# Performance work log

Hardware: AMD Instinct MI355X
Metric: run time of the kernel (lower is better)

## Reference

```python
import jax, jax.numpy as jnp
import numpy as np

N_CAM = 6
N_HEADS = 8
N_POINTS = 4
D = 256  # internal d_model of the deformable attention


def _sine_pos(h, w, d=D):
    # DETR PositionEmbeddingSine, normalize=True, channels-last (h, w, d)
    npf = d // 2
    two_pi = 2.0 * np.pi
    y = jnp.arange(1, h + 1, dtype=jnp.float32) / (h + 1e-6) * two_pi
    x = jnp.arange(1, w + 1, dtype=jnp.float32) / (w + 1e-6) * two_pi
    dim_t = (10000.0 ** (2.0 * (jnp.arange(npf) // 2) / npf)).astype(jnp.float32)
    def enc(v):
        p = v[:, None] / dim_t
        return jnp.stack([jnp.sin(p[:, 0::2]), jnp.cos(p[:, 1::2])], axis=-1).reshape(v.shape[0], -1)
    py, px = enc(y), enc(x)
    return jnp.concatenate([
        jnp.broadcast_to(py[:, None, :], (h, w, npf)),
        jnp.broadcast_to(px[None, :, :], (h, w, npf))], axis=-1)


def _layernorm(x, g, b, eps=1e-5):
    mu = jnp.mean(x, -1, keepdims=True)
    var = jnp.mean((x - mu) ** 2, -1, keepdims=True)
    return (x - mu) * jax.lax.rsqrt(var + eps) * g + b


def _bilinear_gather(kv, loc_x, loc_y, H, W):
    # kv: (b, L, heads, H*W, c); loc_*: (b, Lq, heads, L, P) normalized to [0,1]
    # emulates F.grid_sample(mode='bilinear', padding_mode='zeros', align_corners=False)
    b, L, heads, HW, c = kv.shape
    _, Lq, _, _, P = loc_x.shape
    x = loc_x * W - 0.5
    y = loc_y * H - 0.5
    x0 = jnp.floor(x)
    y0 = jnp.floor(y)
    fx = x - x0
    fy = y - y0
    out = jnp.zeros((b, Lq, heads, L, P, c), kv.dtype)
    for dx in (0, 1):
        for dy in (0, 1):
            xi = x0 + dx
            yi = y0 + dy
            valid = (xi >= 0) & (xi < W) & (yi >= 0) & (yi < H)
            wgt = (fx if dx else 1.0 - fx) * (fy if dy else 1.0 - fy) * valid
            idx = (jnp.clip(yi, 0, H - 1) * W + jnp.clip(xi, 0, W - 1)).astype(jnp.int32)
            idx_t = idx.transpose(0, 3, 2, 1, 4).reshape(b, L, heads, Lq * P, 1)
            g = jnp.take_along_axis(kv, idx_t, axis=3)
            g = g.reshape(b, L, heads, Lq, P, c).transpose(0, 3, 2, 1, 4, 5)
            out = out + wgt[..., None] * g
    return out  # (b, Lq, heads, L, P, c)


def reference(x, conv0_w, conv0_b, conv2_w, conv2_b, cam_emb,
              off_w, off_b, val_w, val_b, key_w, key_b, out_w, out_b,
              conv1_w, conv1_b, norm0_g, norm0_b,
              lin1_w, lin1_b, lin2_w, lin2_b, norm2_g, norm2_b):
    bn, dim, H, W = x.shape
    b = bn // N_CAM
    hd = D // N_HEADS
    HW = H * W
    Lq = N_CAM * HW

    x_nhwc = x.transpose(0, 2, 3, 1)                  # (bn, H, W, dim)
    residual = x_nhwc.reshape(b, Lq, dim)             # b (n h w) d

    src = (x_nhwc @ conv0_w.T + conv0_b).reshape(b, N_CAM, H, W, D)  # conv0 1x1

    pos = _sine_pos(H, W)                              # (H, W, 256)
    spc = src + pos[None, None] + cam_emb[None, :, None, None, :]
    # per-level global descriptor: mean over pixels of conv2(src+pos+cam)
    g = jnp.mean((spc @ conv2_w.T + conv2_b).reshape(b, N_CAM, HW, D), axis=2)  # (b, n, 256)

    src_flat = src.reshape(b, Lq, D)
    query = spc.reshape(b, Lq, D)                      # src + cam + pos (flattened)

    value = src_flat @ val_w.T + val_b
    keys = src_flat @ key_w.T + key_b

    # sampling locations: per-query reference point + learned offsets (normalized)
    offsets = (query @ off_w.T + off_b).reshape(b, Lq, N_HEADS, N_CAM, N_POINTS, 2)
    ry, rx = jnp.meshgrid(
        (jnp.arange(H, dtype=jnp.float32) + 0.5) / H,
        (jnp.arange(W, dtype=jnp.float32) + 0.5) / W, indexing='ij')
    ref = jnp.tile(jnp.stack([rx.ravel(), ry.ravel()], -1), (N_CAM, 1))  # (Lq, 2) as (x, y)
    loc = ref[None, :, None, None, None, :] + offsets / jnp.array([W, H], jnp.float32)

    # gather keys and values in a single bilinear pass (concat on channel)
    kv = jnp.concatenate([
        keys.reshape(b, N_CAM, HW, N_HEADS, hd),
        value.reshape(b, N_CAM, HW, N_HEADS, hd)], axis=-1).transpose(0, 1, 3, 2, 4)
    sampled = _bilinear_gather(kv, loc[..., 0], loc[..., 1], H, W)  # (b,Lq,heads,L,P,2hd)
    k_s, v_s = sampled[..., :hd], sampled[..., hd:]

    # append per-level global token as an extra key/value point per level
    g_h = g.reshape(b, 1, N_CAM, N_HEADS, hd).transpose(0, 1, 3, 2, 4)[:, :, :, :, None, :]
    g_h = jnp.broadcast_to(g_h, (b, Lq, N_HEADS, N_CAM, 1, hd))
    k_all = jnp.concatenate([k_s, g_h], axis=4)        # (b,Lq,heads,L,P+1,hd)
    v_all = jnp.concatenate([v_s, g_h], axis=4)

    # key-aware attention: softmax over all (level, point) sampled keys
    q_h = query.reshape(b, Lq, N_HEADS, hd)
    logits = jnp.einsum('bqhd,bqhlpd->bqhlp', q_h, k_all) / jnp.sqrt(jnp.float32(hd))
    attn = jax.nn.softmax(logits.reshape(b, Lq, N_HEADS, -1), axis=-1).reshape(logits.shape)
    attn_out = jnp.einsum('bqhlp,bqhlpd->bqhd', attn, v_all).reshape(b, Lq, D)
    attn_out = attn_out @ out_w.T + out_b

    out = attn_out @ conv1_w.T + conv1_b               # conv1 1x1 back to dim
    out = _layernorm(residual + out, norm0_g, norm0_b)
    ffn = jax.nn.relu(out @ lin1_w.T + lin1_b) @ lin2_w.T + lin2_b
    out = _layernorm(out + ffn, norm2_g, norm2_b)

    return out.reshape(b, N_CAM, H, W, dim).transpose(0, 1, 4, 2, 3).reshape(bn, dim, H, W)


def setup_inputs() -> dict:
    key = jax.random.key(0)
    ks = jax.random.split(key, 16)
    B, DIM, H, W = 1, 256, 20, 40

    def w(k, shape, s=0.02):
        return jax.random.normal(k, shape, jnp.float32) * s

    n_off = N_HEADS * N_CAM * N_POINTS * 2
    return {
        "x": jax.random.normal(ks[0], (B * N_CAM, DIM, H, W), jnp.float32),
        "conv0_w": w(ks[1], (D, DIM)), "conv0_b": jnp.zeros((D,), jnp.float32),
        "conv2_w": w(ks[2], (D, D)), "conv2_b": jnp.zeros((D,), jnp.float32),
        "cam_emb": jax.random.uniform(ks[3], (N_CAM, D), jnp.float32),
        "off_w": w(ks[4], (n_off, D)),
        "off_b": jax.random.normal(ks[5], (n_off,), jnp.float32) * 0.5,
        "val_w": w(ks[6], (D, D)), "val_b": jnp.zeros((D,), jnp.float32),
        "key_w": w(ks[7], (D, D)), "key_b": jnp.zeros((D,), jnp.float32),
        "out_w": w(ks[8], (D, D)), "out_b": jnp.zeros((D,), jnp.float32),
        "conv1_w": w(ks[9], (DIM, D)), "conv1_b": jnp.zeros((DIM,), jnp.float32),
        "norm0_g": jnp.ones((DIM,), jnp.float32), "norm0_b": jnp.zeros((DIM,), jnp.float32),
        "lin1_w": w(ks[10], (DIM, DIM)), "lin1_b": jnp.zeros((DIM,), jnp.float32),
        "lin2_w": w(ks[11], (DIM, DIM)), "lin2_b": jnp.zeros((DIM,), jnp.float32),
        "norm2_g": jnp.ones((DIM,), jnp.float32), "norm2_b": jnp.zeros((DIM,), jnp.float32),
    }
```

## Files before the change

### kernel.cpp

```cpp
#include <hip/hip_runtime.h>
#include <math.h>

typedef unsigned short u16;
typedef unsigned int u32;

#define NCAM 6
#define NHEADS 8
#define NPOINTS 4
#define DD 256
#define HH 20
#define WW 40
#define HWSZ 800
#define LQ 4800
#define HDIM 32

typedef __attribute__((ext_vector_type(8))) short bf16x8;
typedef __attribute__((ext_vector_type(4))) float f32x4;

__device__ __forceinline__ u16 f2b(float x) {
    union { float f; u32 u; } v;
    v.f = x;
    u32 r = (v.u + 0x7FFFu + ((v.u >> 16) & 1u)) >> 16;
    return (u16)r;
}
__device__ __forceinline__ float lo2f(u32 u) {
    union { u32 u; float f; } v; v.u = u << 16; return v.f;
}
__device__ __forceinline__ float hi2f(u32 u) {
    union { u32 u; float f; } v; v.u = u & 0xFFFF0000u; return v.f;
}

#define P1_BLOCKS 3698
__global__ __launch_bounds__(256) void prep1(
    const float* __restrict__ x, const float* __restrict__ conv0_w,
    const float* __restrict__ conv0_b, const float* __restrict__ key_w,
    const float* __restrict__ key_b, const float* __restrict__ val_w,
    const float* __restrict__ val_b, const float* __restrict__ off_w,
    const float* __restrict__ off_b, const float* __restrict__ lin1_w,
    const float* __restrict__ lin2_w, const float* __restrict__ conv1_w,
    const float* __restrict__ conv1_b, const float* __restrict__ out_w,
    const float* __restrict__ out_b, const float* __restrict__ cam_emb,
    float* __restrict__ pos, u16* __restrict__ xtb, float* __restrict__ mu_x,
    u16* __restrict__ Wcat, float* __restrict__ bias_cat,
    u16* __restrict__ lin1b, u16* __restrict__ lin2b,
    u16* __restrict__ wcombb, float* __restrict__ bcomb,
    float* __restrict__ camoff, float* __restrict__ posy,
    float* __restrict__ posx) {
    int b = blockIdx.x, t = threadIdx.x;
    if (b < 800) {
        int hw = b, d = t;
        int h = hw / WW, w = hw % WW;
        int j = (d & 127) >> 1;
        float dim = powf(10000.0f, (float)j * (1.0f / 64.0f));
        float v;
        if (d < 128) v = (float)(h + 1) / (20.0f + 1e-6f) * (2.0f * (float)M_PI);
        else         v = (float)(w + 1) / (40.0f + 1e-6f) * (2.0f * (float)M_PI);
        float p = v / dim;
        pos[hw * DD + d] = (d & 1) ? cosf(p) : sinf(p);
    } else if (b < 1184) {
        int row = (b - 800) * 4 + (t >> 6);
        int lane = t & 63;
        const float* base = x + (size_t)row * HWSZ;
        float s = 0.f;
        for (int i = lane; i < HWSZ; i += 64) s += base[i];
#pragma unroll
        for (int m = 1; m <= 32; m <<= 1) s += __shfl_xor(s, m);
        if (lane == 0) mu_x[row] = s * (1.0f / (float)HWSZ);
    } else if (b < 1952) {
        int i = (b - 1184) * 256 + t;
        if (i < 65536) {
            Wcat[i] = f2b(conv0_w[i]);
            if (i < 256) bias_cat[i] = conv0_b[i];
        } else if (i < 131072) {
            lin1b[i - 65536] = f2b(lin1_w[i - 65536]);
        } else {
            lin2b[i - 131072] = f2b(lin2_w[i - 131072]);
        }
    } else if (b < 2176) {
        int rbase = 256 + (b - 1952) * 4;
        __shared__ float rowv[4][DD];
        __shared__ float cb[DD];
        cb[t] = conv0_b[t];
#pragma unroll
        for (int j = 0; j < 4; ++j) {
            int row = rbase + j;
            const float* srcp;
            if (row < 768) {
                int rj = row - 256;
                int head = rj >> 6, cpair = (rj >> 1) & 31, kv = rj & 1;
                srcp = (kv ? val_w : key_w) + (size_t)(head * 32 + cpair) * DD;
            } else {
                srcp = off_w + (size_t)(row - 768) * DD;
            }
            rowv[j][t] = srcp[t];
        }
        __syncthreads();
        float acc[4] = {0.f, 0.f, 0.f, 0.f};
        for (int c = 0; c < DD; ++c) {
            float w0 = conv0_w[(size_t)c * DD + t];
#pragma unroll
            for (int j = 0; j < 4; ++j) acc[j] += rowv[j][c] * w0;
        }
#pragma unroll
        for (int j = 0; j < 4; ++j) Wcat[(size_t)(rbase + j) * DD + t] = f2b(acc[j]);
        if (t < 4) {
            int row = rbase + t;
            float bb;
            if (row < 768) {
                int rj = row - 256;
                int head = rj >> 6, cpair = (rj >> 1) & 31, kv = rj & 1;
                bb = (kv ? val_b : key_b)[head * 32 + cpair];
            } else {
                bb = off_b[row - 768];
            }
            for (int c = 0; c < DD; ++c) bb += rowv[t][c] * cb[c];
            bias_cat[row] = bb;
        }
    } else if (b < 2432) {
        int n = b - 2176;
        __shared__ float rowv[DD];
        rowv[t] = conv1_w[(size_t)n * DD + t];
        __syncthreads();
        float acc = 0.f;
        for (int m = 0; m < DD; ++m) acc += rowv[m] * out_w[(size_t)m * DD + t];
        wcombb[(size_t)n * DD + t] = f2b(acc);
        if (t == 0) {
            float bb = conv1_b[n];
            for (int m = 0; m < DD; ++m) bb += rowv[m] * out_b[m];
            bcomb[n] = bb;
        }
    } else if (b < 2438) {
        int cam = b - 2432;
        __shared__ float ce[DD];
        ce[t] = cam_emb[cam * DD + t];
        __syncthreads();
        for (int i = t; i < 384; i += 256) {
            float a = 0.f;
            const float* wr = off_w + (size_t)i * DD;
            for (int c = 0; c < DD; ++c) a += ce[c] * wr[c];
            camoff[cam * 384 + i] = a;
        }
    } else if (b < 2498) {
        int idx = b - 2438;
        __shared__ float pv[128];
        int yside = (idx < 20);
        int coord = yside ? idx : idx - 20;
        if (t < 128) {
            int d = t, j = d >> 1;
            float dim = powf(10000.0f, (float)j * (1.0f / 64.0f));
            float v = yside
                ? (float)(coord + 1) / (20.0f + 1e-6f) * (2.0f * (float)M_PI)
                : (float)(coord + 1) / (40.0f + 1e-6f) * (2.0f * (float)M_PI);
            float p = v / dim;
            pv[d] = (d & 1) ? cosf(p) : sinf(p);
        }
        __syncthreads();
        int koff = yside ? 0 : 128;
        float* outp = yside ? (posy + coord * 384) : (posx + coord * 384);
        for (int n = t; n < 384; n += 256) {
            const float* wr = off_w + (size_t)n * DD + koff;
            float a = 0.f;
            for (int d = 0; d < 128; ++d) a += pv[d] * wr[d];
            outp[n] = a;
        }
    } else {
        int idx = b - 2498;
        int cam = idx / 200, rem = idx % 200;
        int hw0 = (rem % 25) * 32, c0 = (rem / 25) * 32;
        __shared__ float tile[32][33];
        int lhw = t & 31, lc4 = t >> 5;
#pragma unroll
        for (int i = 0; i < 4; ++i) {
            int lc = lc4 * 4 + i;
            tile[lc][lhw] = x[((size_t)(cam * DD + c0 + lc)) * HWSZ + hw0 + lhw];
        }
        __syncthreads();
        int lc2 = t & 31, lhw4 = t >> 5;
#pragma unroll
        for (int i = 0; i < 4; ++i) {
            int lhw2 = lhw4 * 4 + i;
            xtb[((size_t)(cam * HWSZ + hw0 + lhw2)) * DD + c0 + lc2] =
                f2b(tile[lc2][lhw2]);
        }
    }
}

__global__ __launch_bounds__(256) void gemm_fused(
    const u16* __restrict__ Ab, const u16* __restrict__ Wcat,
    const float* __restrict__ bias_cat, const float* __restrict__ pos,
    const float* __restrict__ cam_emb, u16* __restrict__ spcb,
    u16* __restrict__ kvcat16, float* __restrict__ offs,
    const float* __restrict__ mu_x, const float* __restrict__ conv0_w,
    const float* __restrict__ conv0_b, const float* __restrict__ conv2_w,
    const float* __restrict__ conv2_b, float* __restrict__ g) {
    int b = blockIdx.x, t = threadIdx.x;
    if (b < 1350) {
        __shared__ __align__(16) u16 As[1056];
        __shared__ __align__(16) u16 Bs[4120];
        int col0 = (b % 9) * 128, row0 = (b / 9) * 32;
        int wv = t >> 6, lane = t & 63;
        int quad = lane >> 4, l = lane & 15;
        f32x4 acc[2][2] = {};
        for (int k0 = 0; k0 < 256; k0 += 32) {
            __syncthreads();
            if (t < 128) {
                int m = t >> 2, j = t & 3;
                *(uint4*)&As[(j * 33 + m) * 8] =
                    *(const uint4*)&Ab[(size_t)(row0 + m) * 256 + k0 + j * 8];
            }
            {
                int n = t >> 1, jp = (t & 1) * 2;
                const u16* gsrc = &Wcat[(size_t)(col0 + n) * 256 + k0 + jp * 8];
                *(uint4*)&Bs[(jp * 129 + n) * 8]       = *(const uint4*)gsrc;
                *(uint4*)&Bs[((jp + 1) * 129 + n) * 8] = *(const uint4*)(gsrc + 8);
            }
            __syncthreads();
            bf16x8 a0 = *(const bf16x8*)&As[(quad * 33 + l) * 8];
            bf16x8 a1 = *(const bf16x8*)&As[(quad * 33 + 16 + l) * 8];
            bf16x8 b0 = *(const bf16x8*)&Bs[(quad * 129 + wv * 32 + l) * 8];
            bf16x8 b1 = *(const bf16x8*)&Bs[(quad * 129 + wv * 32 + 16 + l) * 8];
            acc[0][0] = __builtin_amdgcn_mfma_f32_16x16x32_bf16(a0, b0, acc[0][0], 0, 0, 0);
            acc[0][1] = __builtin_amdgcn_mfma_f32_16x16x32_bf16(a0, b1, acc[0][1], 0, 0, 0);
            acc[1][0] = __builtin_amdgcn_mfma_f32_16x16x32_bf16(a1, b0, acc[1][0], 0, 0, 0);
            acc[1][1] = __builtin_amdgcn_mfma_f32_16x16x32_bf16(a1, b1, acc[1][1], 0, 0, 0);
        }
#pragma unroll
        for (int mt = 0; mt < 2; ++mt) {
#pragma unroll
            for (int nt = 0; nt < 2; ++nt) {
                int col = col0 + wv * 32 + nt * 16 + l;
                float bb = bias_cat[col];
#pragma unroll
                for (int r = 0; r < 4; ++r) {
                    int row = row0 + mt * 16 + quad * 4 + r;
                    float v = acc[mt][nt][r] + bb;
                    if (col0 < 256) {
                        int cam = row / HWSZ, hw = row % HWSZ;
                        spcb[(size_t)row * 256 + col] =
                            f2b(v + pos[(size_t)hw * 256 + col] + cam_emb[cam * 256 + col]);
                    } else if (col0 < 768) {
                        kvcat16[(size_t)row * 512 + (col - 256)] = f2b(v);
                    } else {
                        offs[(size_t)row * 384 + (col - 768)] = v;
                    }
                }
            }
        }
    } else {
        int cam = b - 1350;
        __shared__ float mu[DD];
        __shared__ float smu[DD];
        float pm;
        {
            int d = t;
            int j = (d & 127) >> 1;
            float inv = 1.0f / powf(10000.0f, (float)j * (1.0f / 64.0f));
            float s = 0.f;
            if (d < 128) {
                for (int h = 0; h < HH; ++h) {
                    float p = (float)(h + 1) / (20.0f + 1e-6f) * (2.0f * (float)M_PI) * inv;
                    s += (d & 1) ? cosf(p) : sinf(p);
                }
                pm = s * (1.0f / (float)HH);
            } else {
                for (int w = 0; w < WW; ++w) {
                    float p = (float)(w + 1) / (40.0f + 1e-6f) * (2.0f * (float)M_PI) * inv;
                    s += (d & 1) ? cosf(p) : sinf(p);
                }
                pm = s * (1.0f / (float)WW);
            }
        }
        mu[t] = mu_x[cam * DD + t];
        __syncthreads();
        float a = conv0_b[t] + pm + cam_emb[cam * DD + t];
        const float* wr = conv0_w + (size_t)t * DD;
        for (int k = 0; k < DD; ++k) a += mu[k] * wr[k];
        smu[t] = a;
        __syncthreads();
        float ga = conv2_b[t];
        const float* w2r = conv2_w + (size_t)t * DD;
        for (int d = 0; d < DD; ++d) ga += smu[d] * w2r[d];
        g[cam * DD + t] = ga;
    }
}

__global__ __launch_bounds__(256, 6) void attn_kernel(
    const u16* __restrict__ spcb, const u16* __restrict__ kvcat16,
    const float* __restrict__ offs, const float* __restrict__ posy,
    const float* __restrict__ posx, const float* __restrict__ camoff,
    const float* __restrict__ g, u16* __restrict__ attn_out) {
    int qq = blockIdx.x;
    int q0 = qq * 2;
    int tid = threadIdx.x;
    int cam = q0 / HWSZ;
    int hw0 = q0 % HWSZ;
    __shared__ float soff[2][384];
    __shared__ float wgt[2][192][4];
    __shared__ int   idxp[2][192][4];
    for (int i = tid; i < 768; i += 256) {
        int qi = i / 384, n = i - qi * 384;
        int hw = hw0 + qi;
        int h = hw / WW, w = hw - h * WW;
        soff[qi][n] = offs[(size_t)(q0 + qi) * 384 + n] + posy[h * 384 + n] +
                      posx[w * 384 + n] + camoff[cam * 384 + n];
    }
    __syncthreads();
    for (int e2 = tid; e2 < 384; e2 += 256) {
        int qi = e2 / 192, e = e2 - qi * 192;
        int head = e / 24, r = e - head * 24;
        int scam = r >> 2;
        int hw = hw0 + qi;
        int h = hw / WW, w = hw - h * WW;
        float X = (float)w + soff[qi][e * 2];
        float Y = (float)h + soff[qi][e * 2 + 1];
        float x0f = floorf(X), y0f = floorf(Y);
        float fx = X - x0f, fy = Y - y0f;
        int x0 = (int)x0f, y0 = (int)y0f, x1 = x0 + 1, y1 = y0 + 1;
        float vx0 = (x0 >= 0 && x0 < WW) ? 1.f : 0.f;
        float vx1 = (x1 >= 0 && x1 < WW) ? 1.f : 0.f;
        float vy0 = (y0 >= 0 && y0 < HH) ? 1.f : 0.f;
        float vy1 = (y1 >= 0 && y1 < HH) ? 1.f : 0.f;
        int cx0 = min(max(x0, 0), WW - 1), cx1 = min(max(x1, 0), WW - 1);
        int cy0 = min(max(y0, 0), HH - 1), cy1 = min(max(y1, 0), HH - 1);
        wgt[qi][e][0] = (1.f - fx) * (1.f - fy) * vx0 * vy0;
        wgt[qi][e][1] = fx * (1.f - fy) * vx1 * vy0;
        wgt[qi][e][2] = (1.f - fx) * fy * vx0 * vy1;
        wgt[qi][e][3] = fx * fy * vx1 * vy1;
        int pb = scam * HWSZ, hb = head * 64;
        idxp[qi][e][0] = ((pb + cy0 * WW + cx0) << 9) + hb;
        idxp[qi][e][1] = ((pb + cy0 * WW + cx1) << 9) + hb;
        idxp[qi][e][2] = ((pb + cy1 * WW + cx0) << 9) + hb;
        idxp[qi][e][3] = ((pb + cy1 * WW + cx1) << 9) + hb;
    }
    __syncthreads();
    int qi = tid >> 7, head = (tid >> 4) & 7, l = tid & 15;
    int q = q0 + qi;
    int c0 = l * 2;
    u32 qu = *(const u32*)&spcb[(size_t)q * 256 + head * 32 + c0];
    const float scale = 0.17677669529663687f;
    float q0s = lo2f(qu) * scale, q1s = hi2f(qu) * scale;
    float m = -1e30f, den = 0.f, o0 = 0.f, o1 = 0.f;
    for (int sc = 0; sc < NCAM; ++sc) {
        float av0[4], av1[4], lg[4];
#pragma unroll
        for (int p = 0; p < 4; ++p) {
            int e = head * 24 + sc * 4 + p;
            float ak0 = 0.f, ak1 = 0.f, a0 = 0.f, a1 = 0.f;
#pragma unroll
            for (int j = 0; j < 4; ++j) {
                float wj = wgt[qi][e][j];
                int idx = idxp[qi][e][j] + 4 * l;
                uint2 d = *(const uint2*)&kvcat16[idx];
                ak0 += wj * lo2f(d.x);
                a0  += wj * hi2f(d.x);
                ak1 += wj * lo2f(d.y);
                a1  += wj * hi2f(d.y);
            }
            av0[p] = a0; av1[p] = a1;
            float pl = q0s * ak0 + q1s * ak1;
            pl += __shfl_xor(pl, 1);
            pl += __shfl_xor(pl, 2);
            pl += __shfl_xor(pl, 4);
            pl += __shfl_xor(pl, 8);
            lg[p] = pl;
        }
        float2 gv = *(const float2*)&g[sc * 256 + head * 32 + c0];
        float pg = q0s * gv.x + q1s * gv.y;
        pg += __shfl_xor(pg, 1);
        pg += __shfl_xor(pg, 2);
        pg += __shfl_xor(pg, 4);
        pg += __shfl_xor(pg, 8);
        float mc = fmaxf(fmaxf(fmaxf(lg[0], lg[1]), fmaxf(lg[2], lg[3])), pg);
        float mn = fmaxf(m, mc);
        float aa = __expf(m - mn);
        float e0p = __expf(lg[0] - mn), e1p = __expf(lg[1] - mn);
        float e2p = __expf(lg[2] - mn), e3p = __expf(lg[3] - mn);
        float e4p = __expf(pg - mn);
        den = den * aa + (e0p + e1p + e2p + e3p + e4p);
        o0 = o0 * aa + e0p * av0[0] + e1p * av0[1] + e2p * av0[2] + e3p * av0[3] + e4p * gv.x;
        o1 = o1 * aa + e0p * av1[0] + e1p * av1[1] + e2p * av1[2] + e3p * av1[3] + e4p * gv.y;
        m = mn;
    }
    float inv = 1.f / den;
    u32 pack = (u32)f2b(o0 * inv) | ((u32)f2b(o1 * inv) << 16);
    *(u32*)&attn_out[(size_t)q * 256 + head * 32 + c0] = pack;
}

__global__ __launch_bounds__(256) void epilogue(
    const u16* __restrict__ Ab, const u16* __restrict__ Wc,
    const float* __restrict__ bcomb, const float* __restrict__ x_nchw,
    const float* __restrict__ n0g, const float* __restrict__ n0b,
    const u16* __restrict__ W1, const float* __restrict__ b1v,
    const u16* __restrict__ W2, const float* __restrict__ b2v,
    const float* __restrict__ n2g, const float* __restrict__ n2b,
    float* __restrict__ out_nchw) {
    __shared__ __align__(16) u16 As[552];
    __shared__ __align__(16) u16 Bs[8232];
    __shared__ __align__(16) u16 A2[4360];
    __shared__ float red[4][4][4][2];
    int t = threadIdx.x;
    int row0 = blockIdx.x * 16;
    int wv = t >> 6, lane = t & 63, quad = lane >> 4, l = lane & 15;
    int cam = row0 / HWSZ;
    int hw0q = row0 % HWSZ + quad * 4;

    f32x4 acc[4] = {};
    for (int k0 = 0; k0 < 256; k0 += 32) {
        __syncthreads();
        if (t < 64) {
            int mm = t >> 2, j = t & 3;
            *(uint4*)&As[(j * 17 + mm) * 8] =
                *(const uint4*)&Ab[(size_t)(row0 + mm) * 256 + k0 + j * 8];
        }
#pragma unroll
        for (int j = 0; j < 4; ++j)
            *(uint4*)&Bs[(j * 257 + t) * 8] =
                *(const uint4*)&Wc[(size_t)t * 256 + k0 + j * 8];
        __syncthreads();
        bf16x8 a = *(const bf16x8*)&As[(quad * 17 + l) * 8];
#pragma unroll
        for (int nt = 0; nt < 4; ++nt) {
            bf16x8 b = *(const bf16x8*)&Bs[(quad * 257 + wv * 64 + nt * 16 + l) * 8];
            acc[nt] = __builtin_amdgcn_mfma_f32_16x16x32_bf16(a, b, acc[nt], 0, 0, 0);
        }
    }
    float v[4][4];
    int cols[4];
#pragma unroll
    for (int nt = 0; nt < 4; ++nt) {
        int col = wv * 64 + nt * 16 + l;
        cols[nt] = col;
        float bb = bcomb[col];
        float4 rx = *(const float4*)&x_nchw[((size_t)(cam * 256 + col)) * HWSZ + hw0q];
        v[nt][0] = acc[nt][0] + bb + rx.x;
        v[nt][1] = acc[nt][1] + bb + rx.y;
        v[nt][2] = acc[nt][2] + bb + rx.z;
        v[nt][3] = acc[nt][3] + bb + rx.w;
    }
#pragma unroll
    for (int r = 0; r < 4; ++r) {
        float s = v[0][r] + v[1][r] + v[2][r] + v[3][r];
        float sq = v[0][r] * v[0][r] + v[1][r] * v[1][r] +
                   v[2][r] * v[2][r] + v[3][r] * v[3][r];
#pragma unroll
        for (int msk = 1; msk <= 8; msk <<= 1) {
            s += __shfl_xor(s, msk);
            sq += __shfl_xor(sq, msk);
        }
        if (l == 0) { red[wv][quad][r][0] = s; red[wv][quad][r][1] = sq; }
    }
    __syncthreads();
    float o0[4][4];
#pragma unroll
    for (int r = 0; r < 4; ++r) {
        float S = red[0][quad][r][0] + red[1][quad][r][0] +
                  red[2][quad][r][0] + red[3][quad][r][0];
        float Q = red[0][quad][r][1] + red[1][quad][r][1] +
                  red[2][quad][r][1] + red[3][quad][r][1];
        float mean = S * (1.0f / 256.0f);
        float var = Q * (1.0f / 256.0f) - mean * mean;
        float rstd = rsqrtf(var + 1e-5f);
        int row = quad * 4 + r;
#pragma unroll
        for (int nt = 0; nt < 4; ++nt) {
            int col = cols[nt];
            float ov = (v[nt][r] - mean) * rstd * n0g[col] + n0b[col];
            o0[nt][r] = ov;
            A2[((col >> 3) * 17 + row) * 8 + (col & 7)] = f2b(ov);
        }
    }
    f32x4 acc2[4] = {};
    for (int k0 = 0; k0 < 256; k0 += 32) {
        __syncthreads();
#pragma unroll
        for (int j = 0; j < 4; ++j)
            *(uint4*)&Bs[(j * 257 + t) * 8] =
                *(const uint4*)&W1[(size_t)t * 256 + k0 + j * 8];
        __syncthreads();
        bf16x8 a = *(const bf16x8*)&A2[(((k0 >> 3) + quad) * 17 + l) * 8];
#pragma unroll
        for (int nt = 0; nt < 4; ++nt) {
            bf16x8 b = *(const bf16x8*)&Bs[(quad * 257 + wv * 64 + nt * 16 + l) * 8];
            acc2[nt] = __builtin_amdgcn_mfma_f32_16x16x32_bf16(a, b, acc2[nt], 0, 0, 0);
        }
    }
    __syncthreads();
#pragma unroll
    for (int nt = 0; nt < 4; ++nt) {
        int col = cols[nt];
        float bb = b1v[col];
#pragma unroll
        for (int r = 0; r < 4; ++r) {
            int row = quad * 4 + r;
            A2[((col >> 3) * 17 + row) * 8 + (col & 7)] = f2b(fmaxf(acc2[nt][r] + bb, 0.f));
        }
    }
    f32x4 acc3[4] = {};
    for (int k0 = 0; k0 < 256; k0 += 32) {
        __syncthreads();
#pragma unroll
        for (int j = 0; j < 4; ++j)
            *(uint4*)&Bs[(j * 257 + t) * 8] =
                *(const uint4*)&W2[(size_t)t * 256 + k0 + j * 8];
        __syncthreads();
        bf16x8 a = *(const bf16x8*)&A2[(((k0 >> 3) + quad) * 17 + l) * 8];
#pragma unroll
        for (int nt = 0; nt < 4; ++nt) {
            bf16x8 b = *(const bf16x8*)&Bs[(quad * 257 + wv * 64 + nt * 16 + l) * 8];
            acc3[nt] = __builtin_amdgcn_mfma_f32_16x16x32_bf16(a, b, acc3[nt], 0, 0, 0);
        }
    }
    float v2[4][4];
#pragma unroll
    for (int nt = 0; nt < 4; ++nt) {
        float bb = b2v[cols[nt]];
#pragma unroll
        for (int r = 0; r < 4; ++r) v2[nt][r] = acc3[nt][r] + bb + o0[nt][r];
    }
    __syncthreads();
#pragma unroll
    for (int r = 0; r < 4; ++r) {
        float s = v2[0][r] + v2[1][r] + v2[2][r] + v2[3][r];
        float sq = v2[0][r] * v2[0][r] + v2[1][r] * v2[1][r] +
                   v2[2][r] * v2[2][r] + v2[3][r] * v2[3][r];
#pragma unroll
        for (int msk = 1; msk <= 8; msk <<= 1) {
            s += __shfl_xor(s, msk);
            sq += __shfl_xor(sq, msk);
        }
        if (l == 0) { red[wv][quad][r][0] = s; red[wv][quad][r][1] = sq; }
    }
    __syncthreads();
    float mean2[4], rstd2[4];
#pragma unroll
    for (int r = 0; r < 4; ++r) {
        float S = red[0][quad][r][0] + red[1][quad][r][0] +
                  red[2][quad][r][0] + red[3][quad][r][0];
        float Q = red[0][quad][r][1] + red[1][quad][r][1] +
                  red[2][quad][r][1] + red[3][quad][r][1];
        mean2[r] = S * (1.0f / 256.0f);
        float var = Q * (1.0f / 256.0f) - mean2[r] * mean2[r];
        rstd2[r] = rsqrtf(var + 1e-5f);
    }
#pragma unroll
    for (int nt = 0; nt < 4; ++nt) {
        int col = cols[nt];
        float gg = n2g[col], bb = n2b[col];
        float4 ov4;
        ov4.x = (v2[nt][0] - mean2[0]) * rstd2[0] * gg + bb;
        ov4.y = (v2[nt][1] - mean2[1]) * rstd2[1] * gg + bb;
        ov4.z = (v2[nt][2] - mean2[2]) * rstd2[2] * gg + bb;
        ov4.w = (v2[nt][3] - mean2[3]) * rstd2[3] * gg + bb;
        *(float4*)&out_nchw[((size_t)(cam * 256 + col)) * HWSZ + hw0q] = ov4;
    }
}

extern "C" void kernel_launch(void* const* d_in, const int* in_sizes, int n_in,
                              void* d_out, int out_size, void* d_ws, size_t ws_size,
                              hipStream_t stream) {
    const float* x       = (const float*)d_in[0];
    const float* conv0_w = (const float*)d_in[1];
    const float* conv0_b = (const float*)d_in[2];
    const float* conv2_w = (const float*)d_in[3];
    const float* conv2_b = (const float*)d_in[4];
    const float* cam_emb = (const float*)d_in[5];
    const float* off_w   = (const float*)d_in[6];
    const float* off_b   = (const float*)d_in[7];
    const float* val_w   = (const float*)d_in[8];
    const float* val_b   = (const float*)d_in[9];
    const float* key_w   = (const float*)d_in[10];
    const float* key_b   = (const float*)d_in[11];
    const float* out_w   = (const float*)d_in[12];
    const float* out_b   = (const float*)d_in[13];
    const float* conv1_w = (const float*)d_in[14];
    const float* conv1_b = (const float*)d_in[15];
    const float* norm0_g = (const float*)d_in[16];
    const float* norm0_b = (const float*)d_in[17];
    const float* lin1_w  = (const float*)d_in[18];
    const float* lin1_b  = (const float*)d_in[19];
    const float* lin2_w  = (const float*)d_in[20];
    const float* lin2_b  = (const float*)d_in[21];
    const float* norm2_g = (const float*)d_in[22];
    const float* norm2_b = (const float*)d_in[23];

    float* ws = (float*)d_ws;
    float* pos      = ws;
    float* mu_x     = pos + 204800;
    float* g        = mu_x + 1536;
    float* camoff   = g + 1536;
    float* posy     = camoff + 2304;
    float* posx     = posy + 7680;
    float* bias_cat = posx + 15360;
    float* bcomb    = bias_cat + 1152;
    float* offs     = bcomb + 256;
    float* f_xtb    = offs + 1843200;
    float* f_spcb   = f_xtb + 614400;
    float* f_kvcat  = f_spcb + 614400;
    float* f_Wcat   = f_kvcat + 1228800;
    float* f_lin1b  = f_Wcat + 147456;
    float* f_lin2b  = f_lin1b + 32768;
    float* f_wcombb = f_lin2b + 32768;

    u16* xtb     = (u16*)f_xtb;
    u16* spcb    = (u16*)f_spcb;
    u16* kvcat16 = (u16*)f_kvcat;
    u16* Wcat    = (u16*)f_Wcat;
    u16* lin1b   = (u16*)f_lin1b;
    u16* lin2b   = (u16*)f_lin2b;
    u16* wcombb  = (u16*)f_wcombb;
    u16* attn_ob = xtb;

    prep1<<<P1_BLOCKS, 256, 0, stream>>>(
        x, conv0_w, conv0_b, key_w, key_b, val_w, val_b, off_w, off_b,
        lin1_w, lin2_w, conv1_w, conv1_b, out_w, out_b, cam_emb,
        pos, xtb, mu_x, Wcat, bias_cat, lin1b, lin2b, wcombb, bcomb,
        camoff, posy, posx);
    gemm_fused<<<1356, 256, 0, stream>>>(xtb, Wcat, bias_cat, pos, cam_emb,
                                         spcb, kvcat16, offs, mu_x, conv0_w,
                                         conv0_b, conv2_w, conv2_b, g);
    attn_kernel<<<LQ / 2, 256, 0, stream>>>(spcb, kvcat16, offs, posy, posx,
                                            camoff, g, attn_ob);
    epilogue<<<300, 256, 0, stream>>>(attn_ob, wcombb, bcomb, x,
                                      norm0_g, norm0_b, lin1b, lin1_b,
                                      lin2b, lin2_b, norm2_g, norm2_b,
                                      (float*)d_out);
}
```

Measured before the change: 220.3 us.

## Move weight folding to MFMA prep kernel, enlarge GEMM tiles, batch attention cameras

Weight folding (key/val/off rows times conv0, and conv1 times out_w) moves out of scalar per-thread loops in prep1 into a new prep2 kernel that uses bf16 MFMA on pre-converted and transposed weights. The small matvecs for camoff, posy/posx and biases now use float4 loads with a 16-lane shuffle reduction. gemm_fused tiles grow from 32 to 64 rows, halving the block count. The attention kernel processes two cameras per online-softmax step with launch bounds lowered to 4 waves, and the folded weights now pass through bf16 before folding, which adds rounding error.

```diff
diff --git a/kernel.cpp b/kernel.cpp
--- a/kernel.cpp
+++ b/kernel.cpp
@@ -29,8 +29,15 @@
 __device__ __forceinline__ float hi2f(u32 u) {
     union { u32 u; float f; } v; v.u = u & 0xFFFF0000u; return v.f;
 }
-
-#define P1_BLOCKS 3698
+__device__ __forceinline__ float red16(float s) {
+    s += __shfl_xor(s, 1);
+    s += __shfl_xor(s, 2);
+    s += __shfl_xor(s, 4);
+    s += __shfl_xor(s, 8);
+    return s;
+}
+
+#define P1_BLOCKS 4570
 __global__ __launch_bounds__(256) void prep1(
     const float* __restrict__ x, const float* __restrict__ conv0_w,
     const float* __restrict__ conv0_b, const float* __restrict__ key_w,
@@ -42,10 +49,12 @@
     const float* __restrict__ out_b, const float* __restrict__ cam_emb,
     float* __restrict__ pos, u16* __restrict__ xtb, float* __restrict__ mu_x,
     u16* __restrict__ Wcat, float* __restrict__ bias_cat,
-    u16* __restrict__ lin1b, u16* __restrict__ lin2b,
-    u16* __restrict__ wcombb, float* __restrict__ bcomb,
-    float* __restrict__ camoff, float* __restrict__ posy,
-    float* __restrict__ posx) {
+    u16* __restrict__ conv1b, u16* __restrict__ lin1b, u16* __restrict__ lin2b,
+    u16* __restrict__ off_wb, u16* __restrict__ kvpackb,
+    u16* __restrict__ conv0_wTb, u16* __restrict__ out_wTb,
+    float* __restrict__ bcomb, float* __restrict__ camoff,
+    float* __restrict__ posy, float* __restrict__ posx) {
+    __shared__ float sbuf[1088];
     int b = blockIdx.x, t = threadIdx.x;
     if (b < 800) {
         int hw = b, d = t;
@@ -66,83 +75,67 @@
 #pragma unroll
         for (int m = 1; m <= 32; m <<= 1) s += __shfl_xor(s, m);
         if (lane == 0) mu_x[row] = s * (1.0f / (float)HWSZ);
-    } else if (b < 1952) {
+    } else if (b < 3104) {
         int i = (b - 1184) * 256 + t;
         if (i < 65536) {
             Wcat[i] = f2b(conv0_w[i]);
             if (i < 256) bias_cat[i] = conv0_b[i];
         } else if (i < 131072) {
-            lin1b[i - 65536] = f2b(lin1_w[i - 65536]);
+            conv1b[i - 65536] = f2b(conv1_w[i - 65536]);
+        } else if (i < 196608) {
+            lin1b[i - 131072] = f2b(lin1_w[i - 131072]);
+        } else if (i < 262144) {
+            lin2b[i - 196608] = f2b(lin2_w[i - 196608]);
+        } else if (i < 360448) {
+            off_wb[i - 262144] = f2b(off_w[i - 262144]);
         } else {
-            lin2b[i - 131072] = f2b(lin2_w[i - 131072]);
-        }
-    } else if (b < 2176) {
-        int rbase = 256 + (b - 1952) * 4;
-        __shared__ float rowv[4][DD];
-        __shared__ float cb[DD];
-        cb[t] = conv0_b[t];
-#pragma unroll
-        for (int j = 0; j < 4; ++j) {
-            int row = rbase + j;
-            const float* srcp;
-            if (row < 768) {
-                int rj = row - 256;
-                int head = rj >> 6, cpair = (rj >> 1) & 31, kv = rj & 1;
-                srcp = (kv ? val_w : key_w) + (size_t)(head * 32 + cpair) * DD;
-            } else {
-                srcp = off_w + (size_t)(row - 768) * DD;
-            }
-            rowv[j][t] = srcp[t];
-        }
-        __syncthreads();
-        float acc[4] = {0.f, 0.f, 0.f, 0.f};
-        for (int c = 0; c < DD; ++c) {
-            float w0 = conv0_w[(size_t)c * DD + t];
-#pragma unroll
-            for (int j = 0; j < 4; ++j) acc[j] += rowv[j][c] * w0;
-        }
-#pragma unroll
-        for (int j = 0; j < 4; ++j) Wcat[(size_t)(rbase + j) * DD + t] = f2b(acc[j]);
-        if (t < 4) {
-            int row = rbase + t;
-            float bb;
-            if (row < 768) {
-                int rj = row - 256;
-                int head = rj >> 6, cpair = (rj >> 1) & 31, kv = rj & 1;
-                bb = (kv ? val_b : key_b)[head * 32 + cpair];
-            } else {
-                bb = off_b[row - 768];
-            }
-            for (int c = 0; c < DD; ++c) bb += rowv[t][c] * cb[c];
-            bias_cat[row] = bb;
-        }
-    } else if (b < 2432) {
-        int n = b - 2176;
-        __shared__ float rowv[DD];
-        rowv[t] = conv1_w[(size_t)n * DD + t];
-        __syncthreads();
-        float acc = 0.f;
-        for (int m = 0; m < DD; ++m) acc += rowv[m] * out_w[(size_t)m * DD + t];
-        wcombb[(size_t)n * DD + t] = f2b(acc);
-        if (t == 0) {
-            float bb = conv1_b[n];
-            for (int m = 0; m < DD; ++m) bb += rowv[m] * out_b[m];
-            bcomb[n] = bb;
-        }
-    } else if (b < 2438) {
-        int cam = b - 2432;
-        __shared__ float ce[DD];
-        ce[t] = cam_emb[cam * DD + t];
-        __syncthreads();
-        for (int i = t; i < 384; i += 256) {
-            float a = 0.f;
-            const float* wr = off_w + (size_t)i * DD;
-            for (int c = 0; c < DD; ++c) a += ce[c] * wr[c];
-            camoff[cam * 384 + i] = a;
-        }
-    } else if (b < 2498) {
-        int idx = b - 2438;
-        __shared__ float pv[128];
+            int j = i - 360448;
+            int rj = j >> 8, k = j & 255;
+            int head = rj >> 6, cpair = (rj >> 1) & 31, kv = rj & 1;
+            kvpackb[j] = f2b((kv ? val_w : key_w)[(size_t)(head * 32 + cpair) * 256 + k]);
+        }
+    } else if (b < 3232) {
+        int idx = b - 3104;
+        int which = idx >> 6;
+        int t2 = idx & 63;
+        int k0 = (t2 >> 3) * 32, c0 = (t2 & 7) * 32;
+        const float* src = which ? out_w : conv0_w;
+        u16* dst = which ? out_wTb : conv0_wTb;
+        float (*tile)[33] = (float(*)[33])sbuf;
+        int lc = t & 31, lk4 = t >> 5;
+#pragma unroll
+        for (int i = 0; i < 4; ++i) {
+            int lk = lk4 * 4 + i;
+            tile[lk][lc] = src[(size_t)(k0 + lk) * 256 + c0 + lc];
+        }
+        __syncthreads();
+        int lk2 = t & 31, lc4 = t >> 5;
+#pragma unroll
+        for (int i = 0; i < 4; ++i) {
+            int lc2 = lc4 * 4 + i;
+            dst[(size_t)(c0 + lc2) * 256 + k0 + lk2] = f2b(tile[lk2][lc2]);
+        }
+    } else if (b < 4432) {
+        int idx = b - 3232;
+        int cam = idx / 200, rem = idx % 200;
+        int hw0 = (rem % 25) * 32, c0 = (rem / 25) * 32;
+        float (*tile)[33] = (float(*)[33])sbuf;
+        int lhw = t & 31, lc4 = t >> 5;
+#pragma unroll
+        for (int i = 0; i < 4; ++i) {
+            int lc = lc4 * 4 + i;
+            tile[lc][lhw] = x[((size_t)(cam * DD + c0 + lc)) * HWSZ + hw0 + lhw];
+        }
+        __syncthreads();
+        int lc2 = t & 31, lhw4 = t >> 5;
+#pragma unroll
+        for (int i = 0; i < 4; ++i) {
+            int lhw2 = lhw4 * 4 + i;
+            xtb[((size_t)(cam * HWSZ + hw0 + lhw2)) * DD + c0 + lc2] =
+                f2b(tile[lc2][lhw2]);
+        }
+    } else if (b < 4492) {
+        int idx = b - 4432;
         int yside = (idx < 20);
         int coord = yside ? idx : idx - 20;
         if (t < 128) {
@@ -152,35 +145,138 @@
                 ? (float)(coord + 1) / (20.0f + 1e-6f) * (2.0f * (float)M_PI)
                 : (float)(coord + 1) / (40.0f + 1e-6f) * (2.0f * (float)M_PI);
             float p = v / dim;
-            pv[d] = (d & 1) ? cosf(p) : sinf(p);
+            sbuf[d] = (d & 1) ? cosf(p) : sinf(p);
         }
         __syncthreads();
         int koff = yside ? 0 : 128;
         float* outp = yside ? (posy + coord * 384) : (posx + coord * 384);
-        for (int n = t; n < 384; n += 256) {
-            const float* wr = off_w + (size_t)n * DD + koff;
-            float a = 0.f;
-            for (int d = 0; d < 128; ++d) a += pv[d] * wr[d];
-            outp[n] = a;
-        }
+        int l = t & 15, og = t >> 4;
+#pragma unroll
+        for (int chunk = 0; chunk < 24; ++chunk) {
+            int n = chunk * 16 + og;
+            const float* wr = off_w + (size_t)n * 256 + koff + l * 8;
+            float4 w0 = *(const float4*)wr;
+            float4 w1 = *(const float4*)(wr + 4);
+            const float* pv = sbuf + l * 8;
+            float s = pv[0] * w0.x + pv[1] * w0.y + pv[2] * w0.z + pv[3] * w0.w +
+                      pv[4] * w1.x + pv[5] * w1.y + pv[6] * w1.z + pv[7] * w1.w;
+            s = red16(s);
+            if (l == 0) outp[n] = s;
+        }
+    } else if (b < 4498) {
+        int cam = b - 4492;
+        sbuf[t] = cam_emb[cam * DD + t];
+        __syncthreads();
+        int l = t & 15, og = t >> 4;
+#pragma unroll
+        for (int chunk = 0; chunk < 24; ++chunk) {
+            int n = chunk * 16 + og;
+            const float* wr = off_w + (size_t)n * 256 + l * 16;
+            float s = 0.f;
+#pragma unroll
+            for (int i = 0; i < 4; ++i) {
+                float4 w4 = *(const float4*)(wr + i * 4);
+                const float* ce = sbuf + l * 16 + i * 4;
+                s += ce[0] * w4.x + ce[1] * w4.y + ce[2] * w4.z + ce[3] * w4.w;
+            }
+            s = red16(s);
+            if (l == 0) camoff[cam * 384 + n] = s;
+        }
+    } else if (b < 4554) {
+        sbuf[t] = conv0_b[t];
+        __syncthreads();
+        int l = t & 15, og = t >> 4;
+        int rr = (b - 4498) * 16 + og;
+        const float* srcp;
+        float bsrc;
+        if (rr < 512) {
+            int head = rr >> 6, cpair = (rr >> 1) & 31, kv = rr & 1;
+            srcp = (kv ? val_w : key_w) + (size_t)(head * 32 + cpair) * 256;
+            bsrc = (kv ? val_b : key_b)[head * 32 + cpair];
+        } else {
+            srcp = off_w + (size_t)(rr - 512) * 256;
+            bsrc = off_b[rr - 512];
+        }
+        float s = 0.f;
+#pragma unroll
+        for (int i = 0; i < 4; ++i) {
+            float4 w4 = *(const float4*)(srcp + l * 16 + i * 4);
+            const float* cb = sbuf + l * 16 + i * 4;
+            s += cb[0] * w4.x + cb[1] * w4.y + cb[2] * w4.z + cb[3] * w4.w;
+        }
+        s = red16(s);
+        if (l == 0) bias_cat[256 + rr] = bsrc + s;
     } else {
-        int idx = b - 2498;
-        int cam = idx / 200, rem = idx % 200;
-        int hw0 = (rem % 25) * 32, c0 = (rem / 25) * 32;
-        __shared__ float tile[32][33];
-        int lhw = t & 31, lc4 = t >> 5;
+        sbuf[t] = out_b[t];
+        __syncthreads();
+        int l = t & 15, og = t >> 4;
+        int n = (b - 4554) * 16 + og;
+        float s = 0.f;
 #pragma unroll
         for (int i = 0; i < 4; ++i) {
-            int lc = lc4 * 4 + i;
-            tile[lc][lhw] = x[((size_t)(cam * DD + c0 + lc)) * HWSZ + hw0 + lhw];
-        }
-        __syncthreads();
-        int lc2 = t & 31, lhw4 = t >> 5;
-#pragma unroll
-        for (int i = 0; i < 4; ++i) {
-            int lhw2 = lhw4 * 4 + i;
-            xtb[((size_t)(cam * HWSZ + hw0 + lhw2)) * DD + c0 + lc2] =
-                f2b(tile[lc2][lhw2]);
+            float4 w4 = *(const float4*)(conv1_w + (size_t)n * 256 + l * 16 + i * 4);
+            const float* ob = sbuf + l * 16 + i * 4;
+            s += ob[0] * w4.x + ob[1] * w4.y + ob[2] * w4.z + ob[3] * w4.w;
+        }
+        s = red16(s);
+        if (l == 0) bcomb[n] = conv1_b[n] + s;
+    }
+}
+
+__global__ __launch_bounds__(256) void prep2(
+    const u16* __restrict__ kvpackb, const u16* __restrict__ off_wb,
+    const u16* __restrict__ conv0_wTb, const u16* __restrict__ conv1b,
+    const u16* __restrict__ out_wTb, u16* __restrict__ Wcat,
+    u16* __restrict__ wcombb) {
+    __shared__ __align__(16) u16 As[1056];
+    __shared__ __align__(16) u16 Bs[4120];
+    int b = blockIdx.x, t = threadIdx.x;
+    int isfold = (b < 56);
+    int bb = isfold ? b : b - 56;
+    int row0 = (bb >> 1) * 32, col0 = (bb & 1) * 128;
+    const u16* Wb = isfold ? conv0_wTb : out_wTb;
+    int wv = t >> 6, lane = t & 63;
+    int quad = lane >> 4, l = lane & 15;
+    f32x4 acc[2][2] = {};
+    for (int k0 = 0; k0 < 256; k0 += 32) {
+        __syncthreads();
+        if (t < 128) {
+            int m = t >> 2, j = t & 3;
+            int rr = row0 + m;
+            const u16* ap;
+            if (isfold) ap = (rr < 512) ? (kvpackb + (size_t)rr * 256)
+                                        : (off_wb + (size_t)(rr - 512) * 256);
+            else        ap = conv1b + (size_t)rr * 256;
+            *(uint4*)&As[(j * 33 + m) * 8] = *(const uint4*)&ap[k0 + j * 8];
+        }
+        {
+            int n = t >> 1, jp = (t & 1) * 2;
+            const u16* gsrc = &Wb[(size_t)(col0 + n) * 256 + k0 + jp * 8];
+            *(uint4*)&Bs[(jp * 129 + n) * 8]       = *(const uint4*)gsrc;
+            *(uint4*)&Bs[((jp + 1) * 129 + n) * 8] = *(const uint4*)(gsrc + 8);
+        }
+        __syncthreads();
+        bf16x8 a0 = *(const bf16x8*)&As[(quad * 33 + l) * 8];
+        bf16x8 a1 = *(const bf16x8*)&As[(quad * 33 + 16 + l) * 8];
+        bf16x8 b0 = *(const bf16x8*)&Bs[(quad * 129 + wv * 32 + l) * 8];
+        bf16x8 b1 = *(const bf16x8*)&Bs[(quad * 129 + wv * 32 + 16 + l) * 8];
+        acc[0][0] = __builtin_amdgcn_mfma_f32_16x16x32_bf16(a0, b0, acc[0][0], 0, 0, 0);
+        acc[0][1] = __builtin_amdgcn_mfma_f32_16x16x32_bf16(a0, b1, acc[0][1], 0, 0, 0);
+        acc[1][0] = __builtin_amdgcn_mfma_f32_16x16x32_bf16(a1, b0, acc[1][0], 0, 0, 0);
+        acc[1][1] = __builtin_amdgcn_mfma_f32_16x16x32_bf16(a1, b1, acc[1][1], 0, 0, 0);
+    }
+#pragma unroll
+    for (int mt = 0; mt < 2; ++mt) {
+#pragma unroll
+        for (int nt = 0; nt < 2; ++nt) {
+            int col = col0 + wv * 32 + nt * 16 + l;
+#pragma unroll
+            for (int r = 0; r < 4; ++r) {
+                int rr = row0 + mt * 16 + quad * 4 + r;
+                u16 ov = f2b(acc[mt][nt][r]);
+                if (isfold) Wcat[(size_t)(256 + rr) * 256 + col] = ov;
+                else        wcombb[(size_t)rr * 256 + col] = ov;
+            }
         }
     }
 }
@@ -194,18 +290,18 @@
     const float* __restrict__ conv0_b, const float* __restrict__ conv2_w,
     const float* __restrict__ conv2_b, float* __restrict__ g) {
     int b = blockIdx.x, t = threadIdx.x;
-    if (b < 1350) {
-        __shared__ __align__(16) u16 As[1056];
+    if (b < 675) {
+        __shared__ __align__(16) u16 As[2080];
         __shared__ __align__(16) u16 Bs[4120];
-        int col0 = (b % 9) * 128, row0 = (b / 9) * 32;
+        int col0 = (b % 9) * 128, row0 = (b / 9) * 64;
         int wv = t >> 6, lane = t & 63;
         int quad = lane >> 4, l = lane & 15;
-        f32x4 acc[2][2] = {};
+        f32x4 acc[4][2] = {};
         for (int k0 = 0; k0 < 256; k0 += 32) {
             __syncthreads();
-            if (t < 128) {
+            {
                 int m = t >> 2, j = t & 3;
-                *(uint4*)&As[(j * 33 + m) * 8] =
+                *(uint4*)&As[(j * 65 + m) * 8] =
                     *(const uint4*)&Ab[(size_t)(row0 + m) * 256 + k0 + j * 8];
             }
             {
@@ -215,17 +311,17 @@
                 *(uint4*)&Bs[((jp + 1) * 129 + n) * 8] = *(const uint4*)(gsrc + 8);
             }
             __syncthreads();
-            bf16x8 a0 = *(const bf16x8*)&As[(quad * 33 + l) * 8];
-            bf16x8 a1 = *(const bf16x8*)&As[(quad * 33 + 16 + l) * 8];
             bf16x8 b0 = *(const bf16x8*)&Bs[(quad * 129 + wv * 32 + l) * 8];
             bf16x8 b1 = *(const bf16x8*)&Bs[(quad * 129 + wv * 32 + 16 + l) * 8];
-            acc[0][0] = __builtin_amdgcn_mfma_f32_16x16x32_bf16(a0, b0, acc[0][0], 0, 0, 0);
-            acc[0][1] = __builtin_amdgcn_mfma_f32_16x16x32_bf16(a0, b1, acc[0][1], 0, 0, 0);
-            acc[1][0] = __builtin_amdgcn_mfma_f32_16x16x32_bf16(a1, b0, acc[1][0], 0, 0, 0);
-            acc[1][1] = __builtin_amdgcn_mfma_f32_16x16x32_bf16(a1, b1, acc[1][1], 0, 0, 0);
-        }
-#pragma unroll
-        for (int mt = 0; mt < 2; ++mt) {
+#pragma unroll
+            for (int mt = 0; mt < 4; ++mt) {
+                bf16x8 a = *(const bf16x8*)&As[(quad * 65 + mt * 16 + l) * 8];
+                acc[mt][0] = __builtin_amdgcn_mfma_f32_16x16x32_bf16(a, b0, acc[mt][0], 0, 0, 0);
+                acc[mt][1] = __builtin_amdgcn_mfma_f32_16x16x32_bf16(a, b1, acc[mt][1], 0, 0, 0);
+            }
+        }
+#pragma unroll
+        for (int mt = 0; mt < 4; ++mt) {
 #pragma unroll
             for (int nt = 0; nt < 2; ++nt) {
                 int col = col0 + wv * 32 + nt * 16 + l;
@@ -247,7 +343,7 @@
             }
         }
     } else {
-        int cam = b - 1350;
+        int cam = b - 675;
         __shared__ float mu[DD];
         __shared__ float smu[DD];
         float pm;
@@ -284,7 +380,7 @@
     }
 }
 
-__global__ __launch_bounds__(256, 6) void attn_kernel(
+__global__ __launch_bounds__(256, 4) void attn_kernel(
     const u16* __restrict__ spcb, const u16* __restrict__ kvcat16,
     const float* __restrict__ offs, const float* __restrict__ posy,
     const float* __restrict__ posx, const float* __restrict__ camoff,
@@ -340,16 +436,18 @@
     const float scale = 0.17677669529663687f;
     float q0s = lo2f(qu) * scale, q1s = hi2f(qu) * scale;
     float m = -1e30f, den = 0.f, o0 = 0.f, o1 = 0.f;
-    for (int sc = 0; sc < NCAM; ++sc) {
-        float av0[4], av1[4], lg[4];
-#pragma unroll
-        for (int p = 0; p < 4; ++p) {
-            int e = head * 24 + sc * 4 + p;
+    int l4 = 4 * l;
+    for (int scp = 0; scp < 3; ++scp) {
+        int e0i = head * 24 + scp * 8;
+        float av0[8], av1[8], lg[8];
+#pragma unroll
+        for (int p = 0; p < 8; ++p) {
+            int e = e0i + p;
             float ak0 = 0.f, ak1 = 0.f, a0 = 0.f, a1 = 0.f;
 #pragma unroll
             for (int j = 0; j < 4; ++j) {
                 float wj = wgt[qi][e][j];
-                int idx = idxp[qi][e][j] + 4 * l;
+                int idx = idxp[qi][e][j] + l4;
                 uint2 d = *(const uint2*)&kvcat16[idx];
                 ak0 += wj * lo2f(d.x);
                 a0  += wj * hi2f(d.x);
@@ -358,27 +456,33 @@
             }
             av0[p] = a0; av1[p] = a1;
             float pl = q0s * ak0 + q1s * ak1;
-            pl += __shfl_xor(pl, 1);
-            pl += __shfl_xor(pl, 2);
-            pl += __shfl_xor(pl, 4);
-            pl += __shfl_xor(pl, 8);
-            lg[p] = pl;
-        }
-        float2 gv = *(const float2*)&g[sc * 256 + head * 32 + c0];
-        float pg = q0s * gv.x + q1s * gv.y;
-        pg += __shfl_xor(pg, 1);
-        pg += __shfl_xor(pg, 2);
-        pg += __shfl_xor(pg, 4);
-        pg += __shfl_xor(pg, 8);
-        float mc = fmaxf(fmaxf(fmaxf(lg[0], lg[1]), fmaxf(lg[2], lg[3])), pg);
+            lg[p] = red16(pl);
+        }
+        float2 gva = *(const float2*)&g[(scp * 2) * 256 + head * 32 + c0];
+        float2 gvb = *(const float2*)&g[(scp * 2 + 1) * 256 + head * 32 + c0];
+        float pga = red16(q0s * gva.x + q1s * gva.y);
+        float pgb = red16(q0s * gvb.x + q1s * gvb.y);
+        float mc = fmaxf(pga, pgb);
+#pragma unroll
+        for (int p = 0; p < 8; ++p) mc = fmaxf(mc, lg[p]);
         float mn = fmaxf(m, mc);
         float aa = __expf(m - mn);
-        float e0p = __expf(lg[0] - mn), e1p = __expf(lg[1] - mn);
-        float e2p = __expf(lg[2] - mn), e3p = __expf(lg[3] - mn);
-        float e4p = __expf(pg - mn);
-        den = den * aa + (e0p + e1p + e2p + e3p + e4p);
-        o0 = o0 * aa + e0p * av0[0] + e1p * av0[1] + e2p * av0[2] + e3p * av0[3] + e4p * gv.x;
-        o1 = o1 * aa + e0p * av1[0] + e1p * av1[1] + e2p * av1[2] + e3p * av1[3] + e4p * gv.y;
+        float ee[8];
+        float dsum = 0.f, s0 = 0.f, s1 = 0.f;
+#pragma unroll
+        for (int p = 0; p < 8; ++p) {
+            ee[p] = __expf(lg[p] - mn);
+            dsum += ee[p];
+            s0 += ee[p] * av0[p];
+            s1 += ee[p] * av1[p];
+        }
+        float ea = __expf(pga - mn), eb = __expf(pgb - mn);
+        dsum += ea + eb;
+        s0 += ea * gva.x + eb * gvb.x;
+        s1 += ea * gva.y + eb * gvb.y;
+        den = den * aa + dsum;
+        o0 = o0 * aa + s0;
+        o1 = o1 * aa + s1;
         m = mn;
     }
     float inv = 1.f / den;
@@ -584,6 +688,7 @@
     const float* norm2_b = (const float*)d_in[23];
 
     float* ws = (float*)d_ws;
+    const size_t SZ = (size_t)LQ * DD;
     float* pos      = ws;
     float* mu_x     = pos + 204800;
     float* g        = mu_x + 1536;
@@ -600,24 +705,36 @@
     float* f_lin1b  = f_Wcat + 147456;
     float* f_lin2b  = f_lin1b + 32768;
     float* f_wcombb = f_lin2b + 32768;
-
-    u16* xtb     = (u16*)f_xtb;
-    u16* spcb    = (u16*)f_spcb;
-    u16* kvcat16 = (u16*)f_kvcat;
-    u16* Wcat    = (u16*)f_Wcat;
-    u16* lin1b   = (u16*)f_lin1b;
-    u16* lin2b   = (u16*)f_lin2b;
-    u16* wcombb  = (u16*)f_wcombb;
-    u16* attn_ob = xtb;
+    float* f_conv1b = f_wcombb + 32768;
+    float* f_off_wb = f_conv1b + 32768;
+    float* f_kvpack = f_off_wb + 49152;
+    float* f_c0T    = f_kvpack + 65536;
+    float* f_outT   = f_c0T + 32768;
+
+    u16* xtb      = (u16*)f_xtb;
+    u16* spcb     = (u16*)f_spcb;
+    u16* kvcat16  = (u16*)f_kvcat;
+    u16* Wcat     = (u16*)f_Wcat;
+    u16* lin1b    = (u16*)f_lin1b;
+    u16* lin2b    = (u16*)f_lin2b;
+    u16* wcombb   = (u16*)f_wcombb;
+    u16* conv1b   = (u16*)f_conv1b;
+    u16* off_wb   = (u16*)f_off_wb;
+    u16* kvpackb  = (u16*)f_kvpack;
+    u16* conv0_wTb= (u16*)f_c0T;
+    u16* out_wTb  = (u16*)f_outT;
+    u16* attn_ob  = xtb;
 
     prep1<<<P1_BLOCKS, 256, 0, stream>>>(
         x, conv0_w, conv0_b, key_w, key_b, val_w, val_b, off_w, off_b,
         lin1_w, lin2_w, conv1_w, conv1_b, out_w, out_b, cam_emb,
-        pos, xtb, mu_x, Wcat, bias_cat, lin1b, lin2b, wcombb, bcomb,
-        camoff, posy, posx);
-    gemm_fused<<<1356, 256, 0, stream>>>(xtb, Wcat, bias_cat, pos, cam_emb,
-                                         spcb, kvcat16, offs, mu_x, conv0_w,
-                                         conv0_b, conv2_w, conv2_b, g);
+        pos, xtb, mu_x, Wcat, bias_cat, conv1b, lin1b, lin2b,
+        off_wb, kvpackb, conv0_wTb, out_wTb, bcomb, camoff, posy, posx);
+    prep2<<<72, 256, 0, stream>>>(kvpackb, off_wb, conv0_wTb, conv1b, out_wTb,
+                                  Wcat, wcombb);
+    gemm_fused<<<681, 256, 0, stream>>>(xtb, Wcat, bias_cat, pos, cam_emb,
+                                        spcb, kvcat16, offs, mu_x, conv0_w,
+                                        conv0_b, conv2_w, conv2_b, g);
     attn_kernel<<<LQ / 2, 256, 0, stream>>>(spcb, kvcat16, offs, posy, posx,
                                             camoff, g, attn_ob);
     epilogue<<<300, 256, 0, stream>>>(attn_ob, wcombb, bcomb, x,
```

After: 215.4 us. 2.2% less time.
